# Optimization experiments

Measured on AMD Instinct MI355X. Metric: run time of the kernel, lower is better.

Reference implementation:

```python
import jax, jax.numpy as jnp
import numpy as np

N = 100000      # nodes
E = 1600000     # edges (avg degree 16)
FEAT, HID, OUT = 128, 64, 40
P_DROP = 0.5


def setup_inputs() -> dict:
    key = jax.random.key(0)
    ks = jax.random.split(key, 7)
    x = jax.random.normal(ks[0], (N, FEAT), dtype=jnp.float32)
    edge_index = jax.random.randint(ks[1], (2, E), 0, N, dtype=jnp.int32)
    W1 = jax.random.normal(ks[2], (FEAT, HID), dtype=jnp.float32) / np.float32(np.sqrt(FEAT))
    b1 = jnp.zeros((HID,), jnp.float32)
    W2 = jax.random.normal(ks[3], (HID, OUT), dtype=jnp.float32) / np.float32(np.sqrt(HID))
    b2 = jnp.zeros((OUT,), jnp.float32)
    # scaled inverted-dropout mask: values in {0, 1/(1-p)}
    keep = jax.random.bernoulli(ks[4], 1.0 - P_DROP, (N, HID))
    drop_mask = keep.astype(jnp.float32) / np.float32(1.0 - P_DROP)
    return {"x": x, "edge_index": edge_index, "W1": W1, "b1": b1,
            "W2": W2, "b2": b2, "drop_mask": drop_mask}


def _gcn_conv(x, W, b, src, dst):
    """PyG GCNConv: h = xW; add self-loops; sym-normalized scatter-add; +b."""
    h = x @ W                                   # [N, D_out]
    ones = jnp.ones((src.shape[0],), h.dtype)
    deg = jax.ops.segment_sum(ones, dst, num_segments=N) + 1.0  # +1 self-loop
    dinv = jax.lax.rsqrt(deg)                   # deg > 0 due to self-loops
    norm = dinv[src] * dinv[dst]                # [E]
    msg = h[src] * norm[:, None]                # gather + scale
    agg = jax.ops.segment_sum(msg, dst, num_segments=N)
    agg = agg + h * (dinv * dinv)[:, None]      # self-loop contribution
    return agg + b


def reference(x, edge_index, W1, b1, W2, b2, drop_mask):
    src, dst = edge_index[0], edge_index[1]
    h = _gcn_conv(x, W1, b1, src, dst)
    h = jax.nn.relu(h)
    h = h * drop_mask                           # F.dropout (pre-drawn mask)
    out = _gcn_conv(h, W2, b2, src, dst)
    return out
```

## Files before the change

kernel.cpp:

```cpp
#include <hip/hip_runtime.h>
#include <hip/hip_fp16.h>

#define NN     100000
#define NE     1600000
#define FEAT   128
#define HID    64
#define OUTD   40
#define BNODES 32
#define NSB    ((NN + 255) / 256)
#define NBAGG  (NSB * 8)
#define CAP    5120
#define CCHUNK 2048
#define WSCALE 262144.0f
#define WINV   (1.0f / 262144.0f)

typedef _Float16 half8 __attribute__((ext_vector_type(8)));
typedef float    f32x4 __attribute__((ext_vector_type(4)));

__global__ __launch_bounds__(256) void k_pairs(const int* __restrict__ src,
                                               const int* __restrict__ dst,
                                               int* __restrict__ bfill,
                                               int* __restrict__ pairs) {
    __shared__ int bcnt[NSB];
    __shared__ int gb[NSB];
    int t = threadIdx.x;
    for (int i = t; i < NSB; i += 256) bcnt[i] = 0;
    __syncthreads();
    int e0 = blockIdx.x * CCHUNK;
    int pk[8], bb[8], off[8];
    #pragma unroll
    for (int i = 0; i < 8; ++i) {
        int e = e0 + i * 256 + t;
        if (e < NE) {
            int d = dst[e];
            pk[i]  = (src[e] << 8) | (d & 255);
            bb[i]  = d >> 8;
            off[i] = atomicAdd(&bcnt[bb[i]], 1);
        } else bb[i] = -1;
    }
    __syncthreads();
    for (int i = t; i < NSB; i += 256) {
        int c = bcnt[i];
        gb[i] = c ? (i * CAP + atomicAdd(&bfill[i], c)) : 0;
    }
    __syncthreads();
    #pragma unroll
    for (int i = 0; i < 8; ++i)
        if (bb[i] >= 0) pairs[gb[bb[i]] + off[i]] = pk[i];
}

__global__ __launch_bounds__(256) void k_csr(const int* __restrict__ pairs,
                                             const int* __restrict__ bfill,
                                             int* __restrict__ sb_beg,
                                             int* __restrict__ sb_cnt,
                                             int* __restrict__ csr,
                                             float* __restrict__ dinv) {
    __shared__ int hist[2048];
    __shared__ int exs[2048];
    __shared__ int nd[256];
    __shared__ int part[256];
    __shared__ int poff[9];
    __shared__ int sstart[8];
    __shared__ int dtot[8];
    int b = blockIdx.x, t = threadIdx.x;
    #pragma unroll
    for (int k = 0; k < 8; ++k) hist[t * 8 + k] = 0;
    nd[t] = 0;
    __syncthreads();
    int base = b * CAP, count = bfill[b];
    for (int i = t; i < count; i += 256) {
        int p = pairs[base + i];
        int key = (((p & 255) >> 5) << 8) | ((p >> 17) & 255);
        atomicAdd(&hist[key], 1);
        atomicAdd(&nd[p & 255], 1);
    }
    __syncthreads();
    {
        int node = (b << 8) + t;
        if (node < NN) dinv[node] = rsqrtf((float)nd[t] + 1.0f);
    }
    int loc[8], s0 = 0;
    #pragma unroll
    for (int k = 0; k < 8; ++k) { loc[k] = s0; s0 += hist[t * 8 + k]; }
    part[t] = s0;
    __syncthreads();
    for (int off = 1; off < 256; off <<= 1) {
        int u = (t >= off) ? part[t - off] : 0;
        __syncthreads();
        part[t] += u;
        __syncthreads();
    }
    int pex = part[t] - s0;
    #pragma unroll
    for (int k = 0; k < 8; ++k) exs[t * 8 + k] = pex + loc[k];
    __syncthreads();
    if (t < 8) {
        sstart[t] = exs[t * 256];
        int end = (t == 7) ? count : exs[(t + 1) * 256];
        dtot[t] = end - sstart[t];
    }
    __syncthreads();
    if (t == 0) {
        poff[0] = 0;
        for (int d = 0; d < 8; ++d) poff[d + 1] = poff[d] + ((dtot[d] + 31) & ~31);
    }
    __syncthreads();
    #pragma unroll
    for (int k = 0; k < 8; ++k) {
        int key = t * 8 + k;
        int d = key >> 8;
        exs[key] = poff[d] + (exs[key] - sstart[d]);
        hist[key] = 0;
    }
    __syncthreads();
    for (int i = t; i < count; i += 256) {
        int p = pairs[base + i];
        int key = (((p & 255) >> 5) << 8) | ((p >> 17) & 255);
        int pos = exs[key] + atomicAdd(&hist[key], 1);
        csr[base + pos] = ((p >> 8) << 7) | (p & 31);
    }
    for (int d = 0; d < 8; ++d) {
        int padded = (dtot[d] + 31) & ~31;
        for (int i = dtot[d] + t; i < padded; i += 256)
            csr[base + poff[d] + i] = (NN << 7);
    }
    if (t < 8) {
        sb_beg[b * 8 + t] = base + poff[t];
        sb_cnt[b * 8 + t] = (dtot[t] + 31) & ~31;
    }
}

__global__ __launch_bounds__(256) void k_maskbits(const float* __restrict__ mask,
                                                  unsigned long long* __restrict__ mb) {
    int node = blockIdx.x * 4 + (threadIdx.x >> 6);
    if (node >= NN) return;
    int l = threadIdx.x & 63;
    float m = mask[(size_t)node * HID + l];
    unsigned long long bits = __ballot(m != 0.f);
    if (l == 0) mb[node] = bits;
}

__global__ __launch_bounds__(256) void k_wprep(const float* __restrict__ W1,
                                               const float* __restrict__ W2,
                                               _Float16* __restrict__ w1f,
                                               _Float16* __restrict__ w2f,
                                               __half* __restrict__ h1s,
                                               __half* __restrict__ hhs) {
    int t = threadIdx.x;
    for (int it = t; it < 16 * 64; it += 256) {
        int f = it >> 6, l = it & 63;
        int kk = f >> 2, n = f & 3;
        int krow = kk * 32 + (l >> 4) * 8;
        int col  = n * 16 + (l & 15);
        #pragma unroll
        for (int i = 0; i < 8; ++i)
            w1f[it * 8 + i] = (_Float16)W1[(krow + i) * HID + col];
    }
    for (int it = t; it < 6 * 64; it += 256) {
        int f = it >> 6, l = it & 63;
        int kk = f / 3, n = f - kk * 3;
        int krow = kk * 32 + (l >> 4) * 8;
        int col  = n * 16 + (l & 15);
        #pragma unroll
        for (int i = 0; i < 8; ++i)
            w2f[it * 8 + i] = (col < OUTD) ? (_Float16)W2[(krow + i) * OUTD + col]
                                           : (_Float16)0.f;
    }
    if (t < HID) {
        h1s[(size_t)NN * HID + t] = __float2half(0.f);
        hhs[(size_t)NN * HID + t] = __float2half(0.f);
    }
}

__global__ __launch_bounds__(256) void k_mgemm1(const float* __restrict__ x,
                                                const _Float16* __restrict__ w1f,
                                                const float* __restrict__ dinv,
                                                __half* __restrict__ h1s) {
    int wid = (blockIdx.x * 256 + threadIdx.x) >> 6;
    int l = threadIdx.x & 63;
    if (wid >= NN / 16) return;
    half8 bf[4][4];
    #pragma unroll
    for (int kk = 0; kk < 4; ++kk)
        #pragma unroll
        for (int n = 0; n < 4; ++n)
            bf[kk][n] = ((const half8*)w1f)[(kk * 4 + n) * 64 + l];
    f32x4 acc[4] = {};
    int arow = wid * 16 + (l & 15);
    const float* xp = x + (size_t)arow * FEAT + (l >> 4) * 8;
    #pragma unroll
    for (int kk = 0; kk < 4; ++kk) {
        float4 u0 = *(const float4*)(xp + kk * 32);
        float4 u1 = *(const float4*)(xp + kk * 32 + 4);
        half8 af;
        af[0] = (_Float16)u0.x; af[1] = (_Float16)u0.y;
        af[2] = (_Float16)u0.z; af[3] = (_Float16)u0.w;
        af[4] = (_Float16)u1.x; af[5] = (_Float16)u1.y;
        af[6] = (_Float16)u1.z; af[7] = (_Float16)u1.w;
        #pragma unroll
        for (int n = 0; n < 4; ++n)
            acc[n] = __builtin_amdgcn_mfma_f32_16x16x32_f16(af, bf[kk][n], acc[n], 0, 0, 0);
    }
    int orow = wid * 16 + (l >> 4) * 4;
    int ocol = l & 15;
    float dv[4];
    #pragma unroll
    for (int r = 0; r < 4; ++r) dv[r] = dinv[orow + r];
    #pragma unroll
    for (int n = 0; n < 4; ++n)
        #pragma unroll
        for (int r = 0; r < 4; ++r)
            h1s[(size_t)(orow + r) * HID + n * 16 + ocol] = __float2half(acc[n][r] * dv[r]);
}

template<int MODE>
__global__ __launch_bounds__(256) void k_bagg(const int* __restrict__ csr,
                                              const int* __restrict__ sb_beg,
                                              const int* __restrict__ sb_cnt,
                                              const float* __restrict__ dinv,
                                              const __half* __restrict__ feat,
                                              const float* __restrict__ b1,
                                              const unsigned long long* __restrict__ maskbits,
                                              __half* __restrict__ outp,
                                              const _Float16* __restrict__ w2f,
                                              const float* __restrict__ b2,
                                              float* __restrict__ outf) {
    __shared__ int acc[BNODES * HID];
    int t = threadIdx.x, wv = t >> 6, l = t & 63;
    int bb = blockIdx.x;
    int4* a4 = (int4*)acc;
    for (int i = t; i < BNODES * HID / 4; i += 256) a4[i] = make_int4(0, 0, 0, 0);
    __syncthreads();
    int base  = sb_beg[bb];
    int count = sb_cnt[bb];
    int node0 = (bb >> 3) * 256 + (bb & 7) * 32;
    const char* fb = (const char*)feat + ((size_t)l * 2);
    for (int j = wv * 16; j < count; j += 64) {
        int e[16];
        #pragma unroll
        for (int i = 0; i < 16; ++i) e[i] = csr[base + j + i];
        float a[16];
        #pragma unroll
        for (int i = 0; i < 16; ++i)
            a[i] = __half2float(*(const __half*)(fb + (unsigned)(e[i] & ~127)));
        #pragma unroll
        for (int i = 0; i < 16; ++i)
            atomicAdd(&acc[((e[i] & 31) << 6) + l], (int)(a[i] * WSCALE));
    }
    __syncthreads();
    if (MODE == 0) {
        for (int n = wv; n < BNODES; n += 4) {
            int node = node0 + n;
            if (node >= NN) break;
            float di = dinv[node];
            float selfv = __half2float(feat[(size_t)node * HID + l]);
            float vv = ((float)acc[(n << 6) + l] * WINV + selfv) * di;
            vv += b1[l];
            vv = vv > 0.f ? vv : 0.f;
            unsigned long long mb = maskbits[node];
            vv = ((mb >> l) & 1ull) ? vv * 2.0f * di : 0.0f;
            outp[(size_t)node * HID + l] = __float2half(vv);
        }
    } else {
        if (wv < 2) {
            half8 bf[2][3];
            #pragma unroll
            for (int kk = 0; kk < 2; ++kk)
                #pragma unroll
                for (int n = 0; n < 3; ++n)
                    bf[kk][n] = ((const half8*)w2f)[(kk * 3 + n) * 64 + l];
            int lrow = wv * 16 + (l & 15);
            int node = node0 + lrow;
            int srow = node < NN ? node : NN;
            float di = dinv[node < NN ? node : NN - 1];
            int k0 = (l >> 4) * 8;
            half8 af[2];
            #pragma unroll
            for (int kk = 0; kk < 2; ++kk)
                #pragma unroll
                for (int i = 0; i < 8; ++i) {
                    int k = kk * 32 + k0 + i;
                    float v = ((float)acc[(lrow << 6) + k] * WINV
                              + __half2float(feat[(size_t)srow * HID + k])) * di;
                    af[kk][i] = (_Float16)v;
                }
            f32x4 o[3] = {};
            #pragma unroll
            for (int kk = 0; kk < 2; ++kk)
                #pragma unroll
                for (int n = 0; n < 3; ++n)
                    o[n] = __builtin_amdgcn_mfma_f32_16x16x32_f16(af[kk], bf[kk][n], o[n], 0, 0, 0);
            int orow = node0 + wv * 16 + (l >> 4) * 4;
            int ocol = l & 15;
            #pragma unroll
            for (int n = 0; n < 3; ++n) {
                int col = n * 16 + ocol;
                if (col < OUTD) {
                    float bbias = b2[col];
                    #pragma unroll
                    for (int r = 0; r < 4; ++r) {
                        int row = orow + r;
                        if (row < NN)
                            outf[(size_t)row * OUTD + col] = o[n][r] + bbias;
                    }
                }
            }
        }
    }
}

extern "C" void kernel_launch(void* const* d_in, const int* in_sizes, int n_in,
                              void* d_out, int out_size, void* d_ws, size_t ws_size,
                              hipStream_t stream) {
    const float* x    = (const float*)d_in[0];
    const int*   ei   = (const int*)d_in[1];
    const int*   src  = ei;
    const int*   dst  = ei + NE;
    const float* W1   = (const float*)d_in[2];
    const float* b1   = (const float*)d_in[3];
    const float* W2   = (const float*)d_in[4];
    const float* b2   = (const float*)d_in[5];
    const float* mask = (const float*)d_in[6];
    float* out = (float*)d_out;

    char* ws = (char*)d_ws;
    int*      bfill  = (int*)ws;           ws += (size_t)NSB * 4;
    int*      sb_beg = (int*)ws;           ws += (size_t)NBAGG * 4;
    int*      sb_cnt = (int*)ws;           ws += (size_t)NBAGG * 4;
    float*    dinv   = (float*)ws;         ws += (size_t)NN * 4;
    unsigned long long* maskb = (unsigned long long*)ws; ws += (size_t)NN * 8;
    _Float16* w1f    = (_Float16*)ws;      ws += 16 * 64 * 8 * 2;
    _Float16* w2f    = (_Float16*)ws;      ws += 6 * 64 * 8 * 2;
    int*      csr    = (int*)ws;           ws += (size_t)NSB * CAP * 4;
    __half*   h1s    = (__half*)ws;        ws += (size_t)(NN + 1) * HID * 2;
    __half*   hhs    = (__half*)ws;        ws += (size_t)(NN + 1) * HID * 2;
    int*      pairs  = (int*)hhs;

    hipMemsetAsync(bfill, 0, (size_t)NSB * 4, stream);

    k_pairs   <<<(NE + CCHUNK - 1) / CCHUNK, 256, 0, stream>>>(src, dst, bfill, pairs);
    k_csr     <<<NSB, 256, 0, stream>>>(pairs, bfill, sb_beg, sb_cnt, csr, dinv);
    k_maskbits<<<(NN + 3) / 4, 256, 0, stream>>>(mask, maskb);
    k_wprep   <<<1, 256, 0, stream>>>(W1, W2, w1f, w2f, h1s, hhs);

    k_mgemm1  <<<(NN / 16 + 3) / 4, 256, 0, stream>>>(x, w1f, dinv, h1s);
    k_bagg<0> <<<NBAGG, 256, 0, stream>>>(csr, sb_beg, sb_cnt, dinv, h1s, b1, maskb,
                                          hhs, nullptr, nullptr, nullptr);
    k_bagg<1> <<<NBAGG, 256, 0, stream>>>(csr, sb_beg, sb_cnt, dinv, hhs, nullptr, nullptr,
                                          nullptr, w2f, b2, out);
}
```

Baseline: 180.8 us.

## Vectorize edge bucketing, gather half2 per lane, swizzle LDS accumulator, stage MFMA inputs

The pair-bucketing kernel now reads src/dst as int4 and handles 4096 edges per block. The aggregation loop has each lane gather a half2 (two features) from one of two edges at a time, and the shared accumulator uses an XOR swizzle to spread LDS atomics across banks. In layer 2 the normalized aggregate is first written to a padded fp16 LDS tile by all waves, so the MFMA waves read contiguous half8 fragments instead of doing scattered per-element loads. The aim is fewer memory transactions and less LDS bank conflict, at the cost of an extra barrier and more LDS.

Result: slower. 203.2 us (+12.4%).

```diff
diff --git a/kernel.cpp b/kernel.cpp
--- a/kernel.cpp
+++ b/kernel.cpp
@@ -10,9 +10,10 @@
 #define NSB    ((NN + 255) / 256)
 #define NBAGG  (NSB * 8)
 #define CAP    5120
-#define CCHUNK 2048
+#define CCHUNK 4096
 #define WSCALE 262144.0f
 #define WINV   (1.0f / 262144.0f)
+#define SWZ(n, k) (((n) << 6) + ((k) ^ (((n) & 7) << 3)))
 
 typedef _Float16 half8 __attribute__((ext_vector_type(8)));
 typedef float    f32x4 __attribute__((ext_vector_type(4)));
@@ -26,17 +27,22 @@
     int t = threadIdx.x;
     for (int i = t; i < NSB; i += 256) bcnt[i] = 0;
     __syncthreads();
-    int e0 = blockIdx.x * CCHUNK;
-    int pk[8], bb[8], off[8];
-    #pragma unroll
-    for (int i = 0; i < 8; ++i) {
-        int e = e0 + i * 256 + t;
-        if (e < NE) {
-            int d = dst[e];
-            pk[i]  = (src[e] << 8) | (d & 255);
-            bb[i]  = d >> 8;
-            off[i] = atomicAdd(&bcnt[bb[i]], 1);
-        } else bb[i] = -1;
+    const int4* d4p = (const int4*)dst;
+    const int4* s4p = (const int4*)src;
+    int q0 = blockIdx.x * (CCHUNK / 4);
+    int4 dv[4], sv[4];
+    int off[16];
+    #pragma unroll
+    for (int i = 0; i < 4; ++i) {
+        int q = q0 + i * 256 + t;
+        if (q < NE / 4) {
+            dv[i] = d4p[q];
+            sv[i] = s4p[q];
+            off[i*4+0] = atomicAdd(&bcnt[dv[i].x >> 8], 1);
+            off[i*4+1] = atomicAdd(&bcnt[dv[i].y >> 8], 1);
+            off[i*4+2] = atomicAdd(&bcnt[dv[i].z >> 8], 1);
+            off[i*4+3] = atomicAdd(&bcnt[dv[i].w >> 8], 1);
+        } else dv[i].x = -1;
     }
     __syncthreads();
     for (int i = t; i < NSB; i += 256) {
@@ -45,8 +51,14 @@
     }
     __syncthreads();
     #pragma unroll
-    for (int i = 0; i < 8; ++i)
-        if (bb[i] >= 0) pairs[gb[bb[i]] + off[i]] = pk[i];
+    for (int i = 0; i < 4; ++i) {
+        if (dv[i].x >= 0) {
+            pairs[gb[dv[i].x >> 8] + off[i*4+0]] = (sv[i].x << 8) | (dv[i].x & 255);
+            pairs[gb[dv[i].y >> 8] + off[i*4+1]] = (sv[i].y << 8) | (dv[i].y & 255);
+            pairs[gb[dv[i].z >> 8] + off[i*4+2]] = (sv[i].z << 8) | (dv[i].z & 255);
+            pairs[gb[dv[i].w >> 8] + off[i*4+3]] = (sv[i].w << 8) | (dv[i].w & 255);
+        }
+    }
 }
 
 __global__ __launch_bounds__(256) void k_csr(const int* __restrict__ pairs,
@@ -234,27 +246,31 @@
     int base  = sb_beg[bb];
     int count = sb_cnt[bb];
     int node0 = (bb >> 3) * 256 + (bb & 7) * 32;
-    const char* fb = (const char*)feat + ((size_t)l * 2);
+    int sub = l >> 5;
+    int c0  = (l & 31) * 2;
+    const char* fb = (const char*)feat + ((size_t)c0 * 2);
     for (int j = wv * 16; j < count; j += 64) {
-        int e[16];
-        #pragma unroll
-        for (int i = 0; i < 16; ++i) e[i] = csr[base + j + i];
-        float a[16];
-        #pragma unroll
-        for (int i = 0; i < 16; ++i)
-            a[i] = __half2float(*(const __half*)(fb + (unsigned)(e[i] & ~127)));
-        #pragma unroll
-        for (int i = 0; i < 16; ++i)
-            atomicAdd(&acc[((e[i] & 31) << 6) + l], (int)(a[i] * WSCALE));
-    }
-    __syncthreads();
-    if (MODE == 0) {
+        int e[8];
+        #pragma unroll
+        for (int i = 0; i < 8; ++i) e[i] = csr[base + j + 2 * i + sub];
+        #pragma unroll
+        for (int i = 0; i < 8; ++i) {
+            unsigned roff = (unsigned)(e[i] & ~127);
+            __half2 hv = *(const __half2*)(fb + roff);
+            float2 f2 = __half22float2(hv);
+            int dl = e[i] & 31;
+            atomicAdd(&acc[SWZ(dl, c0)],     (int)(f2.x * WSCALE));
+            atomicAdd(&acc[SWZ(dl, c0 + 1)], (int)(f2.y * WSCALE));
+        }
+    }
+    __syncthreads();
+    if constexpr (MODE == 0) {
         for (int n = wv; n < BNODES; n += 4) {
             int node = node0 + n;
             if (node >= NN) break;
             float di = dinv[node];
             float selfv = __half2float(feat[(size_t)node * HID + l]);
-            float vv = ((float)acc[(n << 6) + l] * WINV + selfv) * di;
+            float vv = ((float)acc[SWZ(n, l)] * WINV + selfv) * di;
             vv += b1[l];
             vv = vv > 0.f ? vv : 0.f;
             unsigned long long mb = maskbits[node];
@@ -262,6 +278,18 @@
             outp[(size_t)node * HID + l] = __float2half(vv);
         }
     } else {
+        __shared__ _Float16 aggf[BNODES][72];
+        for (int n = wv; n < BNODES; n += 4) {
+            int node = node0 + n;
+            float v = 0.f;
+            if (node < NN) {
+                float di = dinv[node];
+                float selfv = __half2float(feat[(size_t)node * HID + l]);
+                v = ((float)acc[SWZ(n, l)] * WINV + selfv) * di;
+            }
+            aggf[n][l] = (_Float16)v;
+        }
+        __syncthreads();
         if (wv < 2) {
             half8 bf[2][3];
             #pragma unroll
@@ -270,26 +298,15 @@
                 for (int n = 0; n < 3; ++n)
                     bf[kk][n] = ((const half8*)w2f)[(kk * 3 + n) * 64 + l];
             int lrow = wv * 16 + (l & 15);
-            int node = node0 + lrow;
-            int srow = node < NN ? node : NN;
-            float di = dinv[node < NN ? node : NN - 1];
             int k0 = (l >> 4) * 8;
-            half8 af[2];
-            #pragma unroll
-            for (int kk = 0; kk < 2; ++kk)
-                #pragma unroll
-                for (int i = 0; i < 8; ++i) {
-                    int k = kk * 32 + k0 + i;
-                    float v = ((float)acc[(lrow << 6) + k] * WINV
-                              + __half2float(feat[(size_t)srow * HID + k])) * di;
-                    af[kk][i] = (_Float16)v;
-                }
             f32x4 o[3] = {};
             #pragma unroll
-            for (int kk = 0; kk < 2; ++kk)
+            for (int kk = 0; kk < 2; ++kk) {
+                half8 af = *(const half8*)&aggf[lrow][kk * 32 + k0];
                 #pragma unroll
                 for (int n = 0; n < 3; ++n)
-                    o[n] = __builtin_amdgcn_mfma_f32_16x16x32_f16(af[kk], bf[kk][n], o[n], 0, 0, 0);
+                    o[n] = __builtin_amdgcn_mfma_f32_16x16x32_f16(af, bf[kk][n], o[n], 0, 0, 0);
+            }
             int orow = node0 + wv * 16 + (l >> 4) * 4;
             int ocol = l & 15;
             #pragma unroll
```
